# Kernel tuning notes

Measured on AMD Instinct MI355X. Metric: run time of the kernel, lower is better.

The kernel has to match this reference:

```python
import jax, jax.numpy as jnp
import numpy as np

B, N, D, S, ITERS = 32, 4096, 256, 7, 3
EPS_LN = 1e-5

def _ln(x, g, b):
    m = jnp.mean(x, axis=-1, keepdims=True)
    v = jnp.mean((x - m) ** 2, axis=-1, keepdims=True)
    return g * (x - m) * jax.lax.rsqrt(v + EPS_LN) + b

def setup_inputs() -> dict:
    key = jax.random.key(0)
    ks = jax.random.split(key, 16)
    w = lambda k, shape: (jax.random.normal(k, shape, jnp.float32) * 0.02)
    return {
        "inputs": jax.random.normal(ks[0], (B, N, D), jnp.float32),
        "noise": jax.random.normal(ks[1], (B, S, D), jnp.float32),
        "ln_in_g": jnp.ones((D,), jnp.float32), "ln_in_b": jnp.zeros((D,), jnp.float32),
        "ln_slots_g": jnp.ones((D,), jnp.float32), "ln_slots_b": jnp.zeros((D,), jnp.float32),
        "ln_mlp_g": jnp.ones((D,), jnp.float32), "ln_mlp_b": jnp.zeros((D,), jnp.float32),
        "slots_mu": w(ks[2], (1, 1, D)),
        "slots_sigma": jnp.ones((1, 1, D), jnp.float32),
        "wq": w(ks[3], (D, D)), "bq": jnp.zeros((D,), jnp.float32),
        "wk": w(ks[4], (D, D)), "bk": jnp.zeros((D,), jnp.float32),
        "wv": w(ks[5], (D, D)), "bv": jnp.zeros((D,), jnp.float32),
        "w_ih": w(ks[6], (3 * D, D)), "b_ih": jnp.zeros((3 * D,), jnp.float32),
        "w_hh": w(ks[7], (3 * D, D)), "b_hh": jnp.zeros((3 * D,), jnp.float32),
        "w1": w(ks[8], (2 * D, D)), "b1": jnp.zeros((2 * D,), jnp.float32),
        "w2": w(ks[9], (D, 2 * D)), "b2": jnp.zeros((D,), jnp.float32),
    }

def reference(inputs, noise, ln_in_g, ln_in_b, ln_slots_g, ln_slots_b, ln_mlp_g, ln_mlp_b,
              slots_mu, slots_sigma, wq, bq, wk, bk, wv, bv,
              w_ih, b_ih, w_hh, b_hh, w1, b1, w2, b2):
    x = _ln(inputs, ln_in_g, ln_in_b)                      # [B,N,D]
    sigma = jax.nn.softplus(slots_sigma)
    slots = slots_mu + sigma * noise                       # [B,S,D]
    k = x @ wk.T + bk                                      # [B,N,D]
    v = x @ wv.T + bv                                      # [B,N,D]
    scale = D ** -0.5
    attn = None
    for _ in range(ITERS):
        slots_prev = slots
        q = _ln(slots, ln_slots_g, ln_slots_b) @ wq.T + bq  # [B,S,D]
        logits = jnp.einsum('bsd,bnd->bsn', q, k) * scale   # [B,S,N]
        attn = jax.nn.softmax(logits, axis=1) + 1e-8        # softmax over slots
        attn = attn / jnp.sum(attn, axis=-1, keepdims=True)
        updates = jnp.einsum('bsn,bnd->bsd', attn, v)       # [B,S,D]
        # GRUCell(updates, slots_prev), torch gate order (r, z, n)
        gi = updates @ w_ih.T + b_ih                        # [B,S,3D]
        gh = slots_prev @ w_hh.T + b_hh
        i_r, i_z, i_n = jnp.split(gi, 3, axis=-1)
        h_r, h_z, h_n = jnp.split(gh, 3, axis=-1)
        r = jax.nn.sigmoid(i_r + h_r)
        z = jax.nn.sigmoid(i_z + h_z)
        n = jnp.tanh(i_n + r * h_n)
        slots = (1.0 - z) * n + z * slots_prev
        h = jax.nn.relu(_ln(slots, ln_mlp_g, ln_mlp_b) @ w1.T + b1)
        slots = slots + h @ w2.T + b2
    return slots, jnp.swapaxes(attn, 1, 2)                 # [B,S,D], [B,N,S]
```

## Files before the change

### kernel.cpp

```cpp
#include <hip/hip_runtime.h>
#include <stdint.h>

typedef unsigned short u16;
typedef unsigned int u32;
typedef float f32x4 __attribute__((ext_vector_type(4)));
typedef short short8 __attribute__((ext_vector_type(8)));

#define NBAT 32
#define NSEQ 4096
#define ND 256
#define NSLOT 7
#define NCHUNK 64

__device__ __forceinline__ u32 bf16rne(float f){
  u32 u = __float_as_uint(f);
  u = u + 0x7FFFu + ((u >> 16) & 1u);
  return u >> 16;
}
__device__ __forceinline__ u32 packbf(float a, float b){
  return (bf16rne(a) & 0xFFFFu) | (bf16rne(b) << 16);
}
__device__ __forceinline__ float bflo(u32 u){ return __uint_as_float(u << 16); }
__device__ __forceinline__ float bfhi(u32 u){ return __uint_as_float(u & 0xFFFF0000u); }

__device__ __forceinline__ void gld16(void* lds, const void* g){
  __builtin_amdgcn_global_load_lds(
      (const __attribute__((address_space(1))) u32*)g,
      (__attribute__((address_space(3))) u32*)lds, 16, 0, 0);
}

__global__ __launch_bounds__(256) void k_prep(
    const float* __restrict__ wk, const float* __restrict__ wv,
    const float* __restrict__ bk, const float* __restrict__ bv,
    const float* __restrict__ mu, const float* __restrict__ sig,
    const float* __restrict__ noise,
    const float* __restrict__ w_ih, const float* __restrict__ b_ih,
    const float* __restrict__ w_hh, const float* __restrict__ b_hh,
    const float* __restrict__ w1, const float* __restrict__ w2,
    const float* __restrict__ wq,
    u16* __restrict__ Wkv, float* __restrict__ biaskv, float* __restrict__ slots,
    u16* __restrict__ Wg, u16* __restrict__ w1b, u16* __restrict__ w2b,
    u16* __restrict__ wqb, float* __restrict__ bg){
  const int bid = blockIdx.x, t = threadIdx.x;
  if (bid < 512){
    const float* src = (bid < 256) ? (wk + (size_t)bid*256) : (wv + (size_t)(bid-256)*256);
    Wkv[(size_t)bid*256 + t] = (u16)bf16rne(src[t]);
  } else if (bid == 512){
    biaskv[t] = bk[t];
    biaskv[256 + t] = bv[t];
  } else if (bid < 737){
    int r = bid - 513;
    float sp = logf(1.f + expf(sig[t]));
    slots[(size_t)r*256 + t] = mu[t] + sp * noise[(size_t)r*256 + t];
  } else if (bid < 1761){
    int j = bid - 737;
    u16 a, b;
    if (j < 512){ a = (u16)bf16rne(w_ih[(size_t)j*256 + t]); b = (u16)bf16rne(w_hh[(size_t)j*256 + t]); }
    else if (j < 768){ a = (u16)bf16rne(w_ih[(size_t)j*256 + t]); b = 0; }
    else { a = 0; b = (u16)bf16rne(w_hh[(size_t)(j-256)*256 + t]); }
    Wg[(size_t)j*512 + t] = a;
    Wg[(size_t)j*512 + 256 + t] = b;
  } else if (bid < 2273){
    int j = bid - 1761;
    w1b[(size_t)j*256 + t] = (u16)bf16rne(w1[(size_t)j*256 + t]);
  } else if (bid < 2529){
    int j = bid - 2273;
    w2b[(size_t)j*512 + t]       = (u16)bf16rne(w2[(size_t)j*512 + t]);
    w2b[(size_t)j*512 + 256 + t] = (u16)bf16rne(w2[(size_t)j*512 + 256 + t]);
  } else if (bid < 2785){
    int j = bid - 2529;
    wqb[(size_t)j*256 + t] = (u16)bf16rne(wq[(size_t)j*256 + t]);
  } else {
#pragma unroll
    for (int ii = 0; ii < 4; ++ii){
      int j = ii*256 + t;
      float v;
      if (j < 512) v = b_ih[j] + b_hh[j];
      else if (j < 768) v = b_ih[j];
      else v = b_hh[j - 256];
      bg[j] = v;
    }
  }
}

__global__ __launch_bounds__(256) void k_ln_in(
    const float* __restrict__ x, const float* __restrict__ g, const float* __restrict__ b,
    u16* __restrict__ xo){
  const int row = blockIdx.x*4 + (threadIdx.x >> 6);
  const int lane = threadIdx.x & 63;
  const f32x4 v = *(const f32x4*)(x + (size_t)row*ND + lane*4);
  float s  = v[0]+v[1]+v[2]+v[3];
  float s2 = v[0]*v[0]+v[1]*v[1]+v[2]*v[2]+v[3]*v[3];
#pragma unroll
  for (int m = 1; m < 64; m <<= 1){ s += __shfl_xor(s, m); s2 += __shfl_xor(s2, m); }
  const float mean = s * (1.f/256.f);
  const float var  = s2 * (1.f/256.f) - mean*mean;
  const float rstd = rsqrtf(var + 1e-5f);
  const f32x4 gg = *(const f32x4*)(g + lane*4);
  const f32x4 bb = *(const f32x4*)(b + lane*4);
  float y0 = (v[0]-mean)*rstd*gg[0] + bb[0];
  float y1 = (v[1]-mean)*rstd*gg[1] + bb[1];
  float y2 = (v[2]-mean)*rstd*gg[2] + bb[2];
  float y3 = (v[3]-mean)*rstd*gg[3] + bb[3];
  uint2 o; o.x = packbf(y0, y1); o.y = packbf(y2, y3);
  *(uint2*)(xo + (size_t)row*ND + lane*4) = o;
}

__global__ __launch_bounds__(256) void k_gemm_kv(
    const u16* __restrict__ X, const u16* __restrict__ W,
    const float* __restrict__ biaskv, u16* __restrict__ kv){
  __shared__ __align__(16) u16 At[128*64];
  __shared__ __align__(16) u16 Bt[128*64];
  const int bid = blockIdx.x;
  const int swz = ((bid & 7) << 9) + (bid >> 3);
  const int mb = swz >> 2, nb = swz & 3;
  const int tid = threadIdx.x, w = tid >> 6, lane = tid & 63;
  const int wm = w >> 1, wn = w & 1;
  f32x4 acc[4][4];
#pragma unroll
  for (int a = 0; a < 4; ++a)
#pragma unroll
    for (int c = 0; c < 4; ++c) acc[a][c] = (f32x4){0.f,0.f,0.f,0.f};

  const int cl = lane & 7;
  for (int kt = 0; kt < 4; ++kt){
#pragma unroll
    for (int i = 0; i < 4; ++i){
      int R = w*32 + i*8 + (lane >> 3);
      int c = cl ^ (R & 7);
      gld16(&At[(w*32 + i*8)*64], X + ((size_t)(mb*128 + R))*256 + kt*64 + c*8);
      gld16(&Bt[(w*32 + i*8)*64], W + ((size_t)(nb*128 + R))*256 + kt*64 + c*8);
    }
    __syncthreads();
#pragma unroll
    for (int kk = 0; kk < 2; ++kk){
      short8 xf[4], wf[4];
#pragma unroll
      for (int xi = 0; xi < 4; ++xi){
        int r = wm*64 + xi*16 + (lane & 15);
        int ch = (kk*4 + (lane >> 4)) ^ (r & 7);
        xf[xi] = *(const short8*)&At[r*64 + ch*8];
      }
#pragma unroll
      for (int wi = 0; wi < 4; ++wi){
        int r = wn*64 + wi*16 + (lane & 15);
        int ch = (kk*4 + (lane >> 4)) ^ (r & 7);
        wf[wi] = *(const short8*)&Bt[r*64 + ch*8];
      }
#pragma unroll
      for (int xi = 0; xi < 4; ++xi)
#pragma unroll
        for (int wi = 0; wi < 4; ++wi)
          acc[xi][wi] = __builtin_amdgcn_mfma_f32_16x16x32_bf16(wf[wi], xf[xi], acc[xi][wi], 0, 0, 0);
    }
    __syncthreads();
  }
  f32x4 bias[4];
#pragma unroll
  for (int wi = 0; wi < 4; ++wi)
    bias[wi] = *(const f32x4*)(biaskv + nb*128 + wn*64 + wi*16 + (lane >> 4)*4);
#pragma unroll
  for (int xi = 0; xi < 4; ++xi){
    size_t m = (size_t)mb*128 + wm*64 + xi*16 + (lane & 15);
    u16* dst = kv + m*512 + nb*128 + wn*64 + (lane >> 4)*4;
#pragma unroll
    for (int wi = 0; wi < 4; ++wi){
      f32x4 c = acc[xi][wi];
      uint2 o;
      o.x = packbf(c[0] + bias[wi][0], c[1] + bias[wi][1]);
      o.y = packbf(c[2] + bias[wi][2], c[3] + bias[wi][3]);
      *(uint2*)(dst + wi*16) = o;
    }
  }
}

template<int MODE>
__global__ __launch_bounds__(256) void k_gemm_s(
    const u16* __restrict__ A, const u16* __restrict__ W,
    const float* __restrict__ bias, int nkt,
    float* __restrict__ outf, u16* __restrict__ outb,
    const float* __restrict__ snew, float* __restrict__ out2, int last){
  __shared__ __align__(16) u16 At[2][128*64];
  __shared__ __align__(16) u16 Bt[2][128*64];
  const int nb = blockIdx.x, mb = blockIdx.y;
  const int tid = threadIdx.x, w = tid >> 6, lane = tid & 63;
  const int wm = w >> 1, wn = w & 1;
  const size_t K = (size_t)nkt * 64;
  f32x4 acc[4][4];
#pragma unroll
  for (int a = 0; a < 4; ++a)
#pragma unroll
    for (int c = 0; c < 4; ++c) acc[a][c] = (f32x4){0.f,0.f,0.f,0.f};

  const int cl = lane & 7;
#define STAGE_S(buf, kt)                                                         \
  {                                                                              \
    _Pragma("unroll")                                                            \
    for (int i = 0; i < 4; ++i){                                                 \
      int R = w*32 + i*8 + (lane >> 3);                                          \
      int c = cl ^ (R & 7);                                                      \
      gld16(&At[buf][(w*32 + i*8)*64], A + ((size_t)(mb*128 + R))*K + (kt)*64 + c*8); \
      gld16(&Bt[buf][(w*32 + i*8)*64], W + ((size_t)(nb*128 + R))*K + (kt)*64 + c*8); \
    }                                                                            \
  }
  STAGE_S(0, 0);
  __syncthreads();
  for (int kt = 0; kt < nkt; ++kt){
    const int cur = kt & 1;
    if (kt < nkt - 1) STAGE_S(cur ^ 1, kt + 1);
#pragma unroll
    for (int kk = 0; kk < 2; ++kk){
      short8 xf[4], wf[4];
#pragma unroll
      for (int xi = 0; xi < 4; ++xi){
        int r = wm*64 + xi*16 + (lane & 15);
        int ch = (kk*4 + (lane >> 4)) ^ (r & 7);
        xf[xi] = *(const short8*)&At[cur][r*64 + ch*8];
      }
#pragma unroll
      for (int wi = 0; wi < 4; ++wi){
        int r = wn*64 + wi*16 + (lane & 15);
        int ch = (kk*4 + (lane >> 4)) ^ (r & 7);
        wf[wi] = *(const short8*)&Bt[cur][r*64 + ch*8];
      }
#pragma unroll
      for (int xi = 0; xi < 4; ++xi)
#pragma unroll
        for (int wi = 0; wi < 4; ++wi)
          acc[xi][wi] = __builtin_amdgcn_mfma_f32_16x16x32_bf16(wf[wi], xf[xi], acc[xi][wi], 0, 0, 0);
    }
    __syncthreads();
  }
#undef STAGE_S
  const int LDO = (MODE == 0) ? 1024 : ((MODE == 1) ? 512 : 256);
  f32x4 b4[4];
#pragma unroll
  for (int wi = 0; wi < 4; ++wi)
    b4[wi] = *(const f32x4*)(bias + nb*128 + wn*64 + wi*16 + (lane >> 4)*4);
#pragma unroll
  for (int xi = 0; xi < 4; ++xi){
    const int m = mb*128 + wm*64 + xi*16 + (lane & 15);
    const int colb = nb*128 + wn*64 + (lane >> 4)*4;
#pragma unroll
    for (int wi = 0; wi < 4; ++wi){
      const int col = colb + wi*16;
      f32x4 c = acc[xi][wi] + b4[wi];
      if (MODE == 0){
        *(f32x4*)(outf + (size_t)m*LDO + col) = c;
      } else if (MODE == 1){
        uint2 o;
        o.x = packbf(fmaxf(c[0],0.f), fmaxf(c[1],0.f));
        o.y = packbf(fmaxf(c[2],0.f), fmaxf(c[3],0.f));
        *(uint2*)(outb + (size_t)m*LDO + col) = o;
      } else if (MODE == 2){
        if (m < 224){
          const f32x4 s4 = *(const f32x4*)(snew + (size_t)m*256 + col);
          f32x4 o = c + s4;
          *(f32x4*)(outf + (size_t)m*LDO + col) = o;
          if (last) *(f32x4*)(out2 + (size_t)m*LDO + col) = o;
        }
      }
    }
  }
}

__global__ __launch_bounds__(256) void k_q(
    const float* __restrict__ slots, const float* __restrict__ g, const float* __restrict__ b,
    const u16* __restrict__ wqb, const float* __restrict__ bq, u16* __restrict__ qeffb){
  __shared__ float lnv[256];
  __shared__ float red[8];
  const int r = blockIdx.x, t = threadIdx.x, w = t >> 6, lane = t & 63;
  const float x = slots[(size_t)r*256 + t];
  float s = x, s2 = x*x;
#pragma unroll
  for (int m = 1; m < 64; m <<= 1){ s += __shfl_xor(s, m); s2 += __shfl_xor(s2, m); }
  if ((t & 63) == 0){ red[t >> 6] = s; red[4 + (t >> 6)] = s2; }
  __syncthreads();
  const float ssum = red[0]+red[1]+red[2]+red[3];
  const float qsum = red[4]+red[5]+red[6]+red[7];
  const float mean = ssum*(1.f/256.f);
  const float var  = qsum*(1.f/256.f) - mean*mean;
  const float rstd = rsqrtf(var + 1e-5f);
  lnv[t] = (x - mean)*rstd*g[t] + b[t];
  __syncthreads();
  const f32x4 l4 = *(const f32x4*)&lnv[lane*4];
  for (int jj = 0; jj < 64; jj += 8){
    float sv[8];
#pragma unroll
    for (int u8 = 0; u8 < 8; ++u8){
      const int j = w*64 + jj + u8;
      const uint2 wr = *(const uint2*)(wqb + (size_t)j*256 + lane*4);
      float d = l4[0]*bflo(wr.x);
      d = fmaf(l4[1], bfhi(wr.x), d);
      d = fmaf(l4[2], bflo(wr.y), d);
      d = fmaf(l4[3], bfhi(wr.y), d);
#pragma unroll
      for (int m = 1; m < 64; m <<= 1) d += __shfl_xor(d, m);
      sv[u8] = d;
    }
#pragma unroll
    for (int u8 = 0; u8 < 8; ++u8){
      const int j = w*64 + jj + u8;
      if (lane == u8)
        qeffb[(size_t)r*256 + j] = (u16)bf16rne((sv[u8] + bq[j]) * 0.09016844f);
    }
  }
}

__global__ __launch_bounds__(256) void k_attn(
    const u16* __restrict__ kv, const u16* __restrict__ qb,
    float* __restrict__ attn_out, float* __restrict__ pacc, float* __restrict__ pw){
  __shared__ __align__(16) float accbuf[4][7][256];
  __shared__ __align__(16) float p_lds[4][16][8];
  __shared__ float wsum_lds[4][8];
  const int chunk = blockIdx.x, b = blockIdx.y;
  const int tid = threadIdx.x, w = tid >> 6, lane = tid & 63;
  const int l15 = lane & 15, g = lane >> 4, hi = lane >> 5;
  const size_t bbase = (size_t)b*NSEQ;
  const int nr0 = chunk*64 + w*16;

  short8 qf[8];
  {
    const u16* qrow = qb + ((size_t)b*7 + l15)*256;
#pragma unroll
    for (int ks = 0; ks < 8; ++ks)
      qf[ks] = *(const short8*)(qrow + (ks*4 + g)*8);
  }
  f32x4 z = {0.f,0.f,0.f,0.f};
#pragma unroll
  for (int ks = 0; ks < 8; ++ks){
    const short8 kf = *(const short8*)(kv + (bbase + nr0 + l15)*512 + (ks*4 + g)*8);
    z = __builtin_amdgcn_mfma_f32_16x16x32_bf16(qf[ks], kf, z, 0, 0, 0);
  }
  float zz[4];
#pragma unroll
  for (int j = 0; j < 4; ++j){
    const int s = g*4 + j;
    zz[j] = (s < 7) ? z[j] : -3.0e38f;
  }
  float mx = fmaxf(fmaxf(zz[0], zz[1]), fmaxf(zz[2], zz[3]));
  mx = fmaxf(mx, __shfl_xor(mx, 16));
  float p[4], psum = 0.f;
#pragma unroll
  for (int j = 0; j < 4; ++j){ p[j] = exp2f(zz[j] - mx); psum += p[j]; }
  psum += __shfl_xor(psum, 16);
  const float rs = 1.f / psum;
#pragma unroll
  for (int j = 0; j < 4; ++j) p[j] = fmaf(p[j], rs, 1e-8f);
  float wloc[4] = {0.f,0.f,0.f,0.f};
  if (lane < 32){
    *(f32x4*)&p_lds[w][l15][g*4] = (f32x4){p[0], p[1], p[2], p[3]};
    const size_t arow = (bbase + nr0 + l15)*7;
#pragma unroll
    for (int j = 0; j < 4; ++j){
      const int s = g*4 + j;
      if (s < 7){ attn_out[arow + s] = p[j]; wloc[j] = p[j]; }
    }
  }
  __syncthreads();
  float acc[7][4];
#pragma unroll
  for (int s = 0; s < 7; ++s){ acc[s][0]=acc[s][1]=acc[s][2]=acc[s][3]=0.f; }
#pragma unroll
  for (int it = 0; it < 8; ++it){
    const int rm = it*2 + hi, ro = it*2 + (1 - hi);
    const uint2 va = *(const uint2*)(kv + (bbase + nr0 + rm)*512 + 256 + (size_t)lane*4);
    const uint2 vb = *(const uint2*)(kv + (bbase + nr0 + ro)*512 + 256 + (size_t)lane*4);
    const f32x4 pm0 = *(const f32x4*)&p_lds[w][rm][0];
    const f32x4 pm1 = *(const f32x4*)&p_lds[w][rm][4];
    const f32x4 po0 = *(const f32x4*)&p_lds[w][ro][0];
    const f32x4 po1 = *(const f32x4*)&p_lds[w][ro][4];
    const float pm[7] = {pm0[0],pm0[1],pm0[2],pm0[3],pm1[0],pm1[1],pm1[2]};
    const float po[7] = {po0[0],po0[1],po0[2],po0[3],po1[0],po1[1],po1[2]};
    const float vm0=bflo(va.x), vm1=bfhi(va.x), vm2=bflo(va.y), vm3=bfhi(va.y);
    const float vo0=bflo(vb.x), vo1=bfhi(vb.x), vo2=bflo(vb.y), vo3=bfhi(vb.y);
#pragma unroll
    for (int s = 0; s < 7; ++s){
      acc[s][0] = fmaf(pm[s], vm0, fmaf(po[s], vo0, acc[s][0]));
      acc[s][1] = fmaf(pm[s], vm1, fmaf(po[s], vo1, acc[s][1]));
      acc[s][2] = fmaf(pm[s], vm2, fmaf(po[s], vo2, acc[s][2]));
      acc[s][3] = fmaf(pm[s], vm3, fmaf(po[s], vo3, acc[s][3]));
    }
  }
#pragma unroll
  for (int m = 1; m < 16; m <<= 1){
#pragma unroll
    for (int j = 0; j < 4; ++j) wloc[j] += __shfl_xor(wloc[j], m);
  }
  if (lane < 32 && l15 == 0){
#pragma unroll
    for (int j = 0; j < 4; ++j) wsum_lds[w][g*4 + j] = wloc[j];
  }
  __syncthreads();
#pragma unroll
  for (int s = 0; s < 7; ++s)
    *(f32x4*)&accbuf[w][s][lane*4] = (f32x4){acc[s][0], acc[s][1], acc[s][2], acc[s][3]};
  __syncthreads();
#pragma unroll
  for (int s = 0; s < 7; ++s){
    float sum = accbuf[0][s][tid] + accbuf[1][s][tid] + accbuf[2][s][tid] + accbuf[3][s][tid];
    pacc[((size_t)chunk*NBAT + b)*(NSLOT*256) + s*256 + tid] = sum;
  }
  if (tid < 7)
    pw[((size_t)chunk*NBAT + b)*NSLOT + tid] =
        wsum_lds[0][tid] + wsum_lds[1][tid] + wsum_lds[2][tid] + wsum_lds[3][tid];
}

__global__ __launch_bounds__(256) void k_slotA(
    const float* __restrict__ pacc, const float* __restrict__ pw,
    const float* __restrict__ slots, u16* __restrict__ A2, float* __restrict__ wsum){
  __shared__ float pwb[NCHUNK];
  const int r = blockIdx.x, t = threadIdx.x;
  if (r >= 224){
    A2[(size_t)r*512 + t] = 0;
    A2[(size_t)r*512 + 256 + t] = 0;
    return;
  }
  if (t < NCHUNK) pwb[t] = pw[(size_t)t*224 + r];
  float u = 0.f;
#pragma unroll 8
  for (int c = 0; c < NCHUNK; ++c) u += pacc[(size_t)c*57344 + (size_t)r*256 + t];
  __syncthreads();
  float wst = 0.f;
#pragma unroll
  for (int c = 0; c < NCHUNK; ++c) wst += pwb[c];
  if (t == 0) wsum[r] = wst;
  A2[(size_t)r*512 + t] = (u16)bf16rne(u / wst);
  A2[(size_t)r*512 + 256 + t] = (u16)bf16rne(slots[(size_t)r*256 + t]);
}

__global__ __launch_bounds__(256) void k_slotB(
    const float* __restrict__ gates, const float* __restrict__ slots,
    const float* __restrict__ gm, const float* __restrict__ bm,
    float* __restrict__ snew, u16* __restrict__ lnm){
  __shared__ float red[8];
  const int r = blockIdx.x, t = threadIdx.x;
  if (r >= 224){ lnm[(size_t)r*256 + t] = 0; return; }
  const float g0  = gates[(size_t)r*1024 + t];
  const float g1  = gates[(size_t)r*1024 + 256 + t];
  const float gin = gates[(size_t)r*1024 + 512 + t];
  const float ghn = gates[(size_t)r*1024 + 768 + t];
  const float spv = slots[(size_t)r*256 + t];
  const float rr = 1.f/(1.f + __expf(-g0));
  const float zz = 1.f/(1.f + __expf(-g1));
  float xx = gin + rr*ghn;
  xx = fminf(fmaxf(xx, -15.f), 15.f);
  const float e2 = __expf(2.f*xx);
  const float nn = (e2 - 1.f)/(e2 + 1.f);
  const float sp = (1.f - zz)*nn + zz*spv;
  snew[(size_t)r*256 + t] = sp;
  float s = sp, s2 = sp*sp;
#pragma unroll
  for (int m = 1; m < 64; m <<= 1){ s += __shfl_xor(s, m); s2 += __shfl_xor(s2, m); }
  if ((t & 63) == 0){ red[t >> 6] = s; red[4 + (t >> 6)] = s2; }
  __syncthreads();
  const float ssum = red[0]+red[1]+red[2]+red[3];
  const float qsum = red[4]+red[5]+red[6]+red[7];
  const float mean = ssum*(1.f/256.f);
  const float var  = qsum*(1.f/256.f) - mean*mean;
  const float rstd = rsqrtf(var + 1e-5f);
  lnm[(size_t)r*256 + t] = (u16)bf16rne((sp - mean)*rstd*gm[t] + bm[t]);
}

__global__ __launch_bounds__(256) void k_norm(
    float* __restrict__ attn, const float* __restrict__ wsum_tot){
  size_t i = (size_t)blockIdx.x*256 + threadIdx.x;
  int s = (int)(i % 7);
  int b = (int)(i / (NSEQ*7));
  attn[i] = attn[i] / wsum_tot[b*7 + s];
}

extern "C" void kernel_launch(void* const* d_in, const int* in_sizes, int n_in,
                              void* d_out, int out_size, void* d_ws, size_t ws_size,
                              hipStream_t stream){
  (void)in_sizes; (void)n_in; (void)out_size; (void)ws_size;
  const float* inputs  = (const float*)d_in[0];
  const float* noise   = (const float*)d_in[1];
  const float* ln_in_g = (const float*)d_in[2];
  const float* ln_in_b = (const float*)d_in[3];
  const float* ln_sl_g = (const float*)d_in[4];
  const float* ln_sl_b = (const float*)d_in[5];
  const float* ln_ml_g = (const float*)d_in[6];
  const float* ln_ml_b = (const float*)d_in[7];
  const float* mu      = (const float*)d_in[8];
  const float* sig     = (const float*)d_in[9];
  const float* wq      = (const float*)d_in[10];
  const float* bq      = (const float*)d_in[11];
  const float* wk      = (const float*)d_in[12];
  const float* bk      = (const float*)d_in[13];
  const float* wv      = (const float*)d_in[14];
  const float* bv      = (const float*)d_in[15];
  const float* w_ih    = (const float*)d_in[16];
  const float* b_ih    = (const float*)d_in[17];
  const float* w_hh    = (const float*)d_in[18];
  const float* b_hh    = (const float*)d_in[19];
  const float* w1      = (const float*)d_in[20];
  const float* b1      = (const float*)d_in[21];
  const float* w2      = (const float*)d_in[22];
  const float* b2      = (const float*)d_in[23];

  char* ws = (char*)d_ws;
  u16*   x_bf   = (u16*)(ws);
  u16*   kv     = (u16*)(ws + 67108864);
  char*  paccch = ws + 201326592;
  float* pacc   = (float*)paccch;
  u16*   Wkv    = (u16*)(ws + 216006656);
  u16*   qeffb  = (u16*)(ws + 216268800);
  float* slots  = (float*)(ws + 216530944);
  float* pw     = (float*)(ws + 216760320);
  float* biaskv = (float*)(ws + 216817664);
  float* wsum   = (float*)(ws + 216819712);
  u16*   A2     = (u16*)(ws + 216820736);
  u16*   Wg     = (u16*)(ws + 217082880);
  u16*   w1b    = (u16*)(ws + 218131456);
  u16*   w2b    = (u16*)(ws + 218393600);
  u16*   wqb    = (u16*)(ws + 218655744);
  float* bg     = (float*)(ws + 218786816);

  float* gates  = (float*)(paccch);
  u16*   hb     = (u16*)(paccch + 1048576);
  u16*   lnm    = (u16*)(paccch + 1310720);
  float* snew   = (float*)(paccch + 1572864);

  float* out_slots = (float*)d_out;
  float* attn = (float*)d_out + 57344;

  k_prep<<<2786, 256, 0, stream>>>(wk, wv, bk, bv, mu, sig, noise,
                                   w_ih, b_ih, w_hh, b_hh, w1, w2, wq,
                                   Wkv, biaskv, slots, Wg, w1b, w2b, wqb, bg);
  k_ln_in<<<32768, 256, 0, stream>>>(inputs, ln_in_g, ln_in_b, x_bf);
  k_gemm_kv<<<4096, 256, 0, stream>>>(x_bf, Wkv, biaskv, kv);
  for (int i = 0; i < 3; ++i){
    const int last = (i == 2) ? 1 : 0;
    k_q<<<224, 256, 0, stream>>>(slots, ln_sl_g, ln_sl_b, wqb, bq, qeffb);
    k_attn<<<dim3(NCHUNK, 32), 256, 0, stream>>>(kv, qeffb, attn, pacc, pw);
    k_slotA<<<256, 256, 0, stream>>>(pacc, pw, slots, A2, wsum);
    k_gemm_s<0><<<dim3(8, 2), 256, 0, stream>>>(A2, Wg, bg, 8, gates, nullptr, nullptr, nullptr, 0);
    k_slotB<<<256, 256, 0, stream>>>(gates, slots, ln_ml_g, ln_ml_b, snew, lnm);
    k_gemm_s<1><<<dim3(4, 2), 256, 0, stream>>>(lnm, w1b, b1, 4, nullptr, hb, nullptr, nullptr, 0);
    k_gemm_s<2><<<dim3(2, 2), 256, 0, stream>>>(hb, w2b, b2, 8, slots, nullptr, snew, out_slots, last);
  }
  k_norm<<<3584, 256, 0, stream>>>(attn, wsum);
}
```

Before: 369.1 us.

## Fuse per-iteration slot update chain into one kernel with GEMV dot products

Replaces the slotA, three small MFMA GEMM launches, slotB and the next iteration's q projection with a single 512-thread kernel per slot row. Each row does GRU gates, the MLP and the next-q LayerNorm/projection as wave-reduced GEMVs over bf16 weights held in LDS-free registers. This cuts five launches per iteration plus the intermediate global round-trips and the padding rows. The attention kernel also hoists its V loads ahead of the softmax, and k_q drops its batched reduce/write pattern. The cost is that each of the 224 blocks re-reads every weight matrix, where the MFMA tiled GEMMs shared them across rows.

```diff
diff --git a/kernel.cpp b/kernel.cpp
--- a/kernel.cpp
+++ b/kernel.cpp
@@ -22,6 +22,13 @@
 }
 __device__ __forceinline__ float bflo(u32 u){ return __uint_as_float(u << 16); }
 __device__ __forceinline__ float bfhi(u32 u){ return __uint_as_float(u & 0xFFFF0000u); }
+__device__ __forceinline__ float bfs(short v){ return __uint_as_float(((u32)(unsigned short)v) << 16); }
+
+__device__ __forceinline__ float wred64(float d){
+#pragma unroll
+  for (int m = 1; m < 64; m <<= 1) d += __shfl_xor(d, m);
+  return d;
+}
 
 __device__ __forceinline__ void gld16(void* lds, const void* g){
   __builtin_amdgcn_global_load_lds(
@@ -174,96 +181,6 @@
   }
 }
 
-template<int MODE>
-__global__ __launch_bounds__(256) void k_gemm_s(
-    const u16* __restrict__ A, const u16* __restrict__ W,
-    const float* __restrict__ bias, int nkt,
-    float* __restrict__ outf, u16* __restrict__ outb,
-    const float* __restrict__ snew, float* __restrict__ out2, int last){
-  __shared__ __align__(16) u16 At[2][128*64];
-  __shared__ __align__(16) u16 Bt[2][128*64];
-  const int nb = blockIdx.x, mb = blockIdx.y;
-  const int tid = threadIdx.x, w = tid >> 6, lane = tid & 63;
-  const int wm = w >> 1, wn = w & 1;
-  const size_t K = (size_t)nkt * 64;
-  f32x4 acc[4][4];
-#pragma unroll
-  for (int a = 0; a < 4; ++a)
-#pragma unroll
-    for (int c = 0; c < 4; ++c) acc[a][c] = (f32x4){0.f,0.f,0.f,0.f};
-
-  const int cl = lane & 7;
-#define STAGE_S(buf, kt)                                                         \
-  {                                                                              \
-    _Pragma("unroll")                                                            \
-    for (int i = 0; i < 4; ++i){                                                 \
-      int R = w*32 + i*8 + (lane >> 3);                                          \
-      int c = cl ^ (R & 7);                                                      \
-      gld16(&At[buf][(w*32 + i*8)*64], A + ((size_t)(mb*128 + R))*K + (kt)*64 + c*8); \
-      gld16(&Bt[buf][(w*32 + i*8)*64], W + ((size_t)(nb*128 + R))*K + (kt)*64 + c*8); \
-    }                                                                            \
-  }
-  STAGE_S(0, 0);
-  __syncthreads();
-  for (int kt = 0; kt < nkt; ++kt){
-    const int cur = kt & 1;
-    if (kt < nkt - 1) STAGE_S(cur ^ 1, kt + 1);
-#pragma unroll
-    for (int kk = 0; kk < 2; ++kk){
-      short8 xf[4], wf[4];
-#pragma unroll
-      for (int xi = 0; xi < 4; ++xi){
-        int r = wm*64 + xi*16 + (lane & 15);
-        int ch = (kk*4 + (lane >> 4)) ^ (r & 7);
-        xf[xi] = *(const short8*)&At[cur][r*64 + ch*8];
-      }
-#pragma unroll
-      for (int wi = 0; wi < 4; ++wi){
-        int r = wn*64 + wi*16 + (lane & 15);
-        int ch = (kk*4 + (lane >> 4)) ^ (r & 7);
-        wf[wi] = *(const short8*)&Bt[cur][r*64 + ch*8];
-      }
-#pragma unroll
-      for (int xi = 0; xi < 4; ++xi)
-#pragma unroll
-        for (int wi = 0; wi < 4; ++wi)
-          acc[xi][wi] = __builtin_amdgcn_mfma_f32_16x16x32_bf16(wf[wi], xf[xi], acc[xi][wi], 0, 0, 0);
-    }
-    __syncthreads();
-  }
-#undef STAGE_S
-  const int LDO = (MODE == 0) ? 1024 : ((MODE == 1) ? 512 : 256);
-  f32x4 b4[4];
-#pragma unroll
-  for (int wi = 0; wi < 4; ++wi)
-    b4[wi] = *(const f32x4*)(bias + nb*128 + wn*64 + wi*16 + (lane >> 4)*4);
-#pragma unroll
-  for (int xi = 0; xi < 4; ++xi){
-    const int m = mb*128 + wm*64 + xi*16 + (lane & 15);
-    const int colb = nb*128 + wn*64 + (lane >> 4)*4;
-#pragma unroll
-    for (int wi = 0; wi < 4; ++wi){
-      const int col = colb + wi*16;
-      f32x4 c = acc[xi][wi] + b4[wi];
-      if (MODE == 0){
-        *(f32x4*)(outf + (size_t)m*LDO + col) = c;
-      } else if (MODE == 1){
-        uint2 o;
-        o.x = packbf(fmaxf(c[0],0.f), fmaxf(c[1],0.f));
-        o.y = packbf(fmaxf(c[2],0.f), fmaxf(c[3],0.f));
-        *(uint2*)(outb + (size_t)m*LDO + col) = o;
-      } else if (MODE == 2){
-        if (m < 224){
-          const f32x4 s4 = *(const f32x4*)(snew + (size_t)m*256 + col);
-          f32x4 o = c + s4;
-          *(f32x4*)(outf + (size_t)m*LDO + col) = o;
-          if (last) *(f32x4*)(out2 + (size_t)m*LDO + col) = o;
-        }
-      }
-    }
-  }
-}
-
 __global__ __launch_bounds__(256) void k_q(
     const float* __restrict__ slots, const float* __restrict__ g, const float* __restrict__ b,
     const u16* __restrict__ wqb, const float* __restrict__ bq, u16* __restrict__ qeffb){
@@ -284,26 +201,17 @@
   lnv[t] = (x - mean)*rstd*g[t] + b[t];
   __syncthreads();
   const f32x4 l4 = *(const f32x4*)&lnv[lane*4];
-  for (int jj = 0; jj < 64; jj += 8){
-    float sv[8];
-#pragma unroll
-    for (int u8 = 0; u8 < 8; ++u8){
-      const int j = w*64 + jj + u8;
-      const uint2 wr = *(const uint2*)(wqb + (size_t)j*256 + lane*4);
-      float d = l4[0]*bflo(wr.x);
-      d = fmaf(l4[1], bfhi(wr.x), d);
-      d = fmaf(l4[2], bflo(wr.y), d);
-      d = fmaf(l4[3], bfhi(wr.y), d);
-#pragma unroll
-      for (int m = 1; m < 64; m <<= 1) d += __shfl_xor(d, m);
-      sv[u8] = d;
-    }
-#pragma unroll
-    for (int u8 = 0; u8 < 8; ++u8){
-      const int j = w*64 + jj + u8;
-      if (lane == u8)
-        qeffb[(size_t)r*256 + j] = (u16)bf16rne((sv[u8] + bq[j]) * 0.09016844f);
-    }
+#pragma unroll 4
+  for (int jj = 0; jj < 64; ++jj){
+    const int j = w*64 + jj;
+    const uint2 wr = *(const uint2*)(wqb + (size_t)j*256 + lane*4);
+    float d = l4[0]*bflo(wr.x);
+    d = fmaf(l4[1], bfhi(wr.x), d);
+    d = fmaf(l4[2], bflo(wr.y), d);
+    d = fmaf(l4[3], bfhi(wr.y), d);
+    d = wred64(d);
+    if (lane == 0)
+      qeffb[(size_t)r*256 + j] = (u16)bf16rne((d + bq[j]) * 0.09016844f);
   }
 }
 
@@ -332,6 +240,12 @@
     const short8 kf = *(const short8*)(kv + (bbase + nr0 + l15)*512 + (ks*4 + g)*8);
     z = __builtin_amdgcn_mfma_f32_16x16x32_bf16(qf[ks], kf, z, 0, 0, 0);
   }
+  uint2 va[8], vb[8];
+#pragma unroll
+  for (int it = 0; it < 8; ++it){
+    va[it] = *(const uint2*)(kv + (bbase + nr0 + it*2 + hi)*512 + 256 + (size_t)lane*4);
+    vb[it] = *(const uint2*)(kv + (bbase + nr0 + it*2 + (1 - hi))*512 + 256 + (size_t)lane*4);
+  }
   float zz[4];
 #pragma unroll
   for (int j = 0; j < 4; ++j){
@@ -364,16 +278,14 @@
 #pragma unroll
   for (int it = 0; it < 8; ++it){
     const int rm = it*2 + hi, ro = it*2 + (1 - hi);
-    const uint2 va = *(const uint2*)(kv + (bbase + nr0 + rm)*512 + 256 + (size_t)lane*4);
-    const uint2 vb = *(const uint2*)(kv + (bbase + nr0 + ro)*512 + 256 + (size_t)lane*4);
     const f32x4 pm0 = *(const f32x4*)&p_lds[w][rm][0];
     const f32x4 pm1 = *(const f32x4*)&p_lds[w][rm][4];
     const f32x4 po0 = *(const f32x4*)&p_lds[w][ro][0];
     const f32x4 po1 = *(const f32x4*)&p_lds[w][ro][4];
     const float pm[7] = {pm0[0],pm0[1],pm0[2],pm0[3],pm1[0],pm1[1],pm1[2]};
     const float po[7] = {po0[0],po0[1],po0[2],po0[3],po1[0],po1[1],po1[2]};
-    const float vm0=bflo(va.x), vm1=bfhi(va.x), vm2=bflo(va.y), vm3=bfhi(va.y);
-    const float vo0=bflo(vb.x), vo1=bfhi(vb.x), vo2=bflo(vb.y), vo3=bfhi(vb.y);
+    const float vm0=bflo(va[it].x), vm1=bfhi(va[it].x), vm2=bflo(va[it].y), vm3=bfhi(va[it].y);
+    const float vo0=bflo(vb[it].x), vo1=bfhi(vb[it].x), vo2=bflo(vb[it].y), vo3=bfhi(vb[it].y);
 #pragma unroll
     for (int s = 0; s < 7; ++s){
       acc[s][0] = fmaf(pm[s], vm0, fmaf(po[s], vo0, acc[s][0]));
@@ -406,60 +318,169 @@
         wsum_lds[0][tid] + wsum_lds[1][tid] + wsum_lds[2][tid] + wsum_lds[3][tid];
 }
 
-__global__ __launch_bounds__(256) void k_slotA(
+__global__ __launch_bounds__(512) void k_fused(
     const float* __restrict__ pacc, const float* __restrict__ pw,
-    const float* __restrict__ slots, u16* __restrict__ A2, float* __restrict__ wsum){
+    float* __restrict__ slots,
+    const u16* __restrict__ Wg, const float* __restrict__ bg,
+    const float* __restrict__ gm, const float* __restrict__ bm,
+    const u16* __restrict__ w1b, const float* __restrict__ b1,
+    const u16* __restrict__ w2b, const float* __restrict__ b2,
+    const float* __restrict__ qg, const float* __restrict__ qb2,
+    const u16* __restrict__ wqb, const float* __restrict__ bq,
+    float* __restrict__ wsum, float* __restrict__ out_slots,
+    u16* __restrict__ qeffb, int last){
+  __shared__ __align__(16) float a2[512];
+  __shared__ __align__(16) float gib[1024];
+  __shared__ __align__(16) float lnb[256];
+  __shared__ __align__(16) float hbuf[512];
+  __shared__ __align__(16) float sl2[256];
+  __shared__ float red[16];
   __shared__ float pwb[NCHUNK];
-  const int r = blockIdx.x, t = threadIdx.x;
-  if (r >= 224){
-    A2[(size_t)r*512 + t] = 0;
-    A2[(size_t)r*512 + 256 + t] = 0;
-    return;
-  }
+  const int r = blockIdx.x, t = threadIdx.x, w = t >> 6, lane = t & 63;
+  const int b = r / 7, s = r - b*7;
+
   if (t < NCHUNK) pwb[t] = pw[(size_t)t*224 + r];
   float u = 0.f;
-#pragma unroll 8
-  for (int c = 0; c < NCHUNK; ++c) u += pacc[(size_t)c*57344 + (size_t)r*256 + t];
+  if (t < 256){
+    const float* pb = pacc + (size_t)b*1792 + s*256 + t;
+#pragma unroll 4
+    for (int c = 0; c < NCHUNK; ++c) u += pb[(size_t)c*57344];
+  }
   __syncthreads();
   float wst = 0.f;
 #pragma unroll
   for (int c = 0; c < NCHUNK; ++c) wst += pwb[c];
   if (t == 0) wsum[r] = wst;
-  A2[(size_t)r*512 + t] = (u16)bf16rne(u / wst);
-  A2[(size_t)r*512 + 256 + t] = (u16)bf16rne(slots[(size_t)r*256 + t]);
-}
-
-__global__ __launch_bounds__(256) void k_slotB(
-    const float* __restrict__ gates, const float* __restrict__ slots,
-    const float* __restrict__ gm, const float* __restrict__ bm,
-    float* __restrict__ snew, u16* __restrict__ lnm){
-  __shared__ float red[8];
-  const int r = blockIdx.x, t = threadIdx.x;
-  if (r >= 224){ lnm[(size_t)r*256 + t] = 0; return; }
-  const float g0  = gates[(size_t)r*1024 + t];
-  const float g1  = gates[(size_t)r*1024 + 256 + t];
-  const float gin = gates[(size_t)r*1024 + 512 + t];
-  const float ghn = gates[(size_t)r*1024 + 768 + t];
-  const float spv = slots[(size_t)r*256 + t];
-  const float rr = 1.f/(1.f + __expf(-g0));
-  const float zz = 1.f/(1.f + __expf(-g1));
-  float xx = gin + rr*ghn;
-  xx = fminf(fmaxf(xx, -15.f), 15.f);
-  const float e2 = __expf(2.f*xx);
-  const float nn = (e2 - 1.f)/(e2 + 1.f);
-  const float sp = (1.f - zz)*nn + zz*spv;
-  snew[(size_t)r*256 + t] = sp;
-  float s = sp, s2 = sp*sp;
-#pragma unroll
-  for (int m = 1; m < 64; m <<= 1){ s += __shfl_xor(s, m); s2 += __shfl_xor(s2, m); }
-  if ((t & 63) == 0){ red[t >> 6] = s; red[4 + (t >> 6)] = s2; }
-  __syncthreads();
-  const float ssum = red[0]+red[1]+red[2]+red[3];
-  const float qsum = red[4]+red[5]+red[6]+red[7];
-  const float mean = ssum*(1.f/256.f);
-  const float var  = qsum*(1.f/256.f) - mean*mean;
-  const float rstd = rsqrtf(var + 1e-5f);
-  lnm[(size_t)r*256 + t] = (u16)bf16rne((sp - mean)*rstd*gm[t] + bm[t]);
+  if (t < 256){
+    a2[t] = u / wst;
+    a2[256 + t] = slots[(size_t)r*256 + t];
+  }
+  __syncthreads();
+  float av[8];
+  *(f32x4*)&av[0] = *(const f32x4*)&a2[lane*8];
+  *(f32x4*)&av[4] = *(const f32x4*)&a2[lane*8 + 4];
+#pragma unroll 4
+  for (int jj = 0; jj < 128; ++jj){
+    const int j = w*128 + jj;
+    const short8 wr = *(const short8*)(Wg + (size_t)j*512 + lane*8);
+    float d = av[0]*bfs(wr[0]);
+    d = fmaf(av[1], bfs(wr[1]), d);
+    d = fmaf(av[2], bfs(wr[2]), d);
+    d = fmaf(av[3], bfs(wr[3]), d);
+    d = fmaf(av[4], bfs(wr[4]), d);
+    d = fmaf(av[5], bfs(wr[5]), d);
+    d = fmaf(av[6], bfs(wr[6]), d);
+    d = fmaf(av[7], bfs(wr[7]), d);
+    d = wred64(d);
+    if (lane == 0) gib[j] = d + bg[j];
+  }
+  __syncthreads();
+  float sp = 0.f;
+  if (t < 256){
+    const float g0  = gib[t];
+    const float g1  = gib[256 + t];
+    const float gin = gib[512 + t];
+    const float ghn = gib[768 + t];
+    const float spv = a2[256 + t];
+    const float rr = 1.f/(1.f + __expf(-g0));
+    const float zz = 1.f/(1.f + __expf(-g1));
+    float xx = gin + rr*ghn;
+    xx = fminf(fmaxf(xx, -15.f), 15.f);
+    const float e2 = __expf(2.f*xx);
+    const float nn = (e2 - 1.f)/(e2 + 1.f);
+    sp = (1.f - zz)*nn + zz*spv;
+  }
+  float rs_ = sp, rq_ = sp*sp;
+#pragma unroll
+  for (int m = 1; m < 64; m <<= 1){ rs_ += __shfl_xor(rs_, m); rq_ += __shfl_xor(rq_, m); }
+  if (t < 256 && lane == 0){ red[w] = rs_; red[8 + w] = rq_; }
+  __syncthreads();
+  {
+    const float ssum = red[0]+red[1]+red[2]+red[3];
+    const float qsum = red[8]+red[9]+red[10]+red[11];
+    const float mean = ssum*(1.f/256.f);
+    const float var  = qsum*(1.f/256.f) - mean*mean;
+    const float rstd = rsqrtf(var + 1e-5f);
+    if (t < 256){
+      a2[t] = sp;
+      lnb[t] = (sp - mean)*rstd*gm[t] + bm[t];
+    }
+  }
+  __syncthreads();
+  {
+    const f32x4 l4 = *(const f32x4*)&lnb[lane*4];
+#pragma unroll 4
+    for (int jj = 0; jj < 64; ++jj){
+      const int j = w*64 + jj;
+      const uint2 wr = *(const uint2*)(w1b + (size_t)j*256 + lane*4);
+      float d = l4[0]*bflo(wr.x);
+      d = fmaf(l4[1], bfhi(wr.x), d);
+      d = fmaf(l4[2], bflo(wr.y), d);
+      d = fmaf(l4[3], bfhi(wr.y), d);
+      d = wred64(d);
+      if (lane == 0) hbuf[j] = fmaxf(d + b1[j], 0.f);
+    }
+  }
+  __syncthreads();
+  {
+    float hv[8];
+    *(f32x4*)&hv[0] = *(const f32x4*)&hbuf[lane*8];
+    *(f32x4*)&hv[4] = *(const f32x4*)&hbuf[lane*8 + 4];
+#pragma unroll 4
+    for (int jj = 0; jj < 32; ++jj){
+      const int j = w*32 + jj;
+      const short8 wr = *(const short8*)(w2b + (size_t)j*512 + lane*8);
+      float d = hv[0]*bfs(wr[0]);
+      d = fmaf(hv[1], bfs(wr[1]), d);
+      d = fmaf(hv[2], bfs(wr[2]), d);
+      d = fmaf(hv[3], bfs(wr[3]), d);
+      d = fmaf(hv[4], bfs(wr[4]), d);
+      d = fmaf(hv[5], bfs(wr[5]), d);
+      d = fmaf(hv[6], bfs(wr[6]), d);
+      d = fmaf(hv[7], bfs(wr[7]), d);
+      d = wred64(d);
+      if (lane == 0){
+        const float o = a2[j] + d + b2[j];
+        sl2[j] = o;
+        slots[(size_t)r*256 + j] = o;
+        if (last) out_slots[(size_t)r*256 + j] = o;
+      }
+    }
+  }
+  if (last) return;
+  __syncthreads();
+  {
+    const float x = (t < 256) ? sl2[t] : 0.f;
+    float rsq = x, rqq = x*x;
+#pragma unroll
+    for (int m = 1; m < 64; m <<= 1){ rsq += __shfl_xor(rsq, m); rqq += __shfl_xor(rqq, m); }
+    if (t < 256 && lane == 0){ red[w] = rsq; red[8 + w] = rqq; }
+  }
+  __syncthreads();
+  {
+    const float ssum = red[0]+red[1]+red[2]+red[3];
+    const float qsum = red[8]+red[9]+red[10]+red[11];
+    const float mean = ssum*(1.f/256.f);
+    const float var  = qsum*(1.f/256.f) - mean*mean;
+    const float rstd = rsqrtf(var + 1e-5f);
+    if (t < 256) lnb[t] = (sl2[t] - mean)*rstd*qg[t] + qb2[t];
+  }
+  __syncthreads();
+  {
+    const f32x4 l4 = *(const f32x4*)&lnb[lane*4];
+#pragma unroll 4
+    for (int jj = 0; jj < 32; ++jj){
+      const int j = w*32 + jj;
+      const uint2 wr = *(const uint2*)(wqb + (size_t)j*256 + lane*4);
+      float d = l4[0]*bflo(wr.x);
+      d = fmaf(l4[1], bfhi(wr.x), d);
+      d = fmaf(l4[2], bflo(wr.y), d);
+      d = fmaf(l4[3], bfhi(wr.y), d);
+      d = wred64(d);
+      if (lane == 0)
+        qeffb[(size_t)r*256 + j] = (u16)bf16rne((d + bq[j]) * 0.09016844f);
+    }
+  }
 }
 
 __global__ __launch_bounds__(256) void k_norm(
@@ -502,26 +523,19 @@
   char* ws = (char*)d_ws;
   u16*   x_bf   = (u16*)(ws);
   u16*   kv     = (u16*)(ws + 67108864);
-  char*  paccch = ws + 201326592;
-  float* pacc   = (float*)paccch;
+  float* pacc   = (float*)(ws + 201326592);
   u16*   Wkv    = (u16*)(ws + 216006656);
   u16*   qeffb  = (u16*)(ws + 216268800);
   float* slots  = (float*)(ws + 216530944);
   float* pw     = (float*)(ws + 216760320);
   float* biaskv = (float*)(ws + 216817664);
   float* wsum   = (float*)(ws + 216819712);
-  u16*   A2     = (u16*)(ws + 216820736);
   u16*   Wg     = (u16*)(ws + 217082880);
   u16*   w1b    = (u16*)(ws + 218131456);
   u16*   w2b    = (u16*)(ws + 218393600);
   u16*   wqb    = (u16*)(ws + 218655744);
   float* bg     = (float*)(ws + 218786816);
 
-  float* gates  = (float*)(paccch);
-  u16*   hb     = (u16*)(paccch + 1048576);
-  u16*   lnm    = (u16*)(paccch + 1310720);
-  float* snew   = (float*)(paccch + 1572864);
-
   float* out_slots = (float*)d_out;
   float* attn = (float*)d_out + 57344;
 
@@ -530,15 +544,14 @@
                                    Wkv, biaskv, slots, Wg, w1b, w2b, wqb, bg);
   k_ln_in<<<32768, 256, 0, stream>>>(inputs, ln_in_g, ln_in_b, x_bf);
   k_gemm_kv<<<4096, 256, 0, stream>>>(x_bf, Wkv, biaskv, kv);
+  k_q<<<224, 256, 0, stream>>>(slots, ln_sl_g, ln_sl_b, wqb, bq, qeffb);
   for (int i = 0; i < 3; ++i){
     const int last = (i == 2) ? 1 : 0;
-    k_q<<<224, 256, 0, stream>>>(slots, ln_sl_g, ln_sl_b, wqb, bq, qeffb);
     k_attn<<<dim3(NCHUNK, 32), 256, 0, stream>>>(kv, qeffb, attn, pacc, pw);
-    k_slotA<<<256, 256, 0, stream>>>(pacc, pw, slots, A2, wsum);
-    k_gemm_s<0><<<dim3(8, 2), 256, 0, stream>>>(A2, Wg, bg, 8, gates, nullptr, nullptr, nullptr, 0);
-    k_slotB<<<256, 256, 0, stream>>>(gates, slots, ln_ml_g, ln_ml_b, snew, lnm);
-    k_gemm_s<1><<<dim3(4, 2), 256, 0, stream>>>(lnm, w1b, b1, 4, nullptr, hb, nullptr, nullptr, 0);
-    k_gemm_s<2><<<dim3(2, 2), 256, 0, stream>>>(hb, w2b, b2, 8, slots, nullptr, snew, out_slots, last);
+    k_fused<<<224, 512, 0, stream>>>(pacc, pw, slots, Wg, bg,
+                                     ln_ml_g, ln_ml_b, w1b, b1, w2b, b2,
+                                     ln_sl_g, ln_sl_b, wqb, bq,
+                                     wsum, out_slots, qeffb, last);
   }
   k_norm<<<3584, 256, 0, stream>>>(attn, wsum);
 }
```

New measurement: 710.6 us. 1.93x slower.
